# Optimization experiments

Measured on AMD Instinct MI355X. Metric: run time of the kernel, lower is better.

Reference implementation:

```python
import jax, jax.numpy as jnp
import numpy as np

H = 256
B = 4096          # number of graphs / motifs in batch
NF = 131072       # focal atoms
NR = 262144       # residues
V = 8001          # vocab.size() + 1
TOPK = 5
DIST_THRESH = 6.0


def setup_inputs() -> dict:
    key = jax.random.key(0)
    ks = jax.random.split(key, 12)
    h_ctx_focal = jax.random.normal(ks[0], (NF, H), dtype=jnp.float32)
    pos_ctx_focal = jax.random.normal(ks[1], (NF, 3), dtype=jnp.float32)
    current_wid = jax.random.randint(ks[2], (B,), 0, V)
    current_atoms_batch = jnp.sort(jax.random.randint(ks[3], (NF,), 0, B))
    h_residue = jax.random.normal(ks[4], (NR, H), dtype=jnp.float32)
    residue_pos = jax.random.normal(ks[5], (NR, 3, 3), dtype=jnp.float32)
    amino_acid_batch = jnp.sort(jax.random.randint(ks[6], (NR,), 0, B))
    emb_weight = jax.random.normal(ks[7], (V, H), dtype=jnp.float32) * 0.02
    mlp_w1 = jax.random.normal(ks[8], (3 * H, H), dtype=jnp.float32) * (1.0 / np.sqrt(3 * H))
    mlp_b1 = jnp.zeros((H,), dtype=jnp.float32)
    mlp_w2 = jax.random.normal(ks[9], (H, H), dtype=jnp.float32) * (1.0 / np.sqrt(H))
    mlp_b2 = jnp.zeros((H,), dtype=jnp.float32)
    return {
        'h_ctx_focal': h_ctx_focal, 'pos_ctx_focal': pos_ctx_focal,
        'current_wid': current_wid, 'current_atoms_batch': current_atoms_batch,
        'h_residue': h_residue, 'residue_pos': residue_pos,
        'amino_acid_batch': amino_acid_batch, 'emb_weight': emb_weight,
        'mlp_w1': mlp_w1, 'mlp_b1': mlp_b1, 'mlp_w2': mlp_w2, 'mlp_b2': mlp_b2,
    }


def reference(h_ctx_focal, pos_ctx_focal, current_wid, current_atoms_batch,
              h_residue, residue_pos, amino_acid_batch,
              emb_weight, mlp_w1, mlp_b1, mlp_w2, mlp_b2):
    nB = current_wid.shape[0]
    # scatter_add over focal atoms -> [B, H]
    node_hiddens = jax.ops.segment_sum(h_ctx_focal, current_atoms_batch, num_segments=nB)
    # embedding lookup -> [B, H]
    motif_hiddens = emb_weight[current_wid]
    # scatter_mean of positions -> [B, 3]
    pos_sum = jax.ops.segment_sum(pos_ctx_focal, current_atoms_batch, num_segments=nB)
    counts = jax.ops.segment_sum(jnp.ones((pos_ctx_focal.shape[0],), jnp.float32),
                                 current_atoms_batch, num_segments=nB)
    center_pos = pos_sum / jnp.maximum(counts, 1.0)[:, None]
    # CA position of each residue, distance mask (< 6 A from motif center)
    ca_pos = residue_pos[:, 1, :]                                  # [NR, 3]
    dist = jnp.linalg.norm(ca_pos - center_pos[amino_acid_batch], axis=1)
    mask = dist < DIST_THRESH                                      # [NR]
    # masked scatter_add of residue embeddings -> [B, H]
    residue_emb = jax.ops.segment_sum(jnp.where(mask[:, None], h_residue, 0.0),
                                      amino_acid_batch, num_segments=nB)
    # motif MLP (2 layers) + projection onto embedding table
    pred_vecs = jnp.concatenate([node_hiddens, motif_hiddens, residue_emb], axis=-1)  # [B, 3H]
    h = jax.nn.relu(pred_vecs @ mlp_w1 + mlp_b1)
    mh = h @ mlp_w2 + mlp_b2                                        # [B, H]
    pred_scores = mh @ emb_weight.T                                 # [B, V]
    # top-k + random selection among top-k
    _, select_pool = jax.lax.top_k(pred_scores, TOPK)               # [B, k]
    idx = jax.random.randint(jax.random.key(1), (nB,), 0, TOPK)
    preds = jnp.take_along_axis(select_pool, idx[:, None], axis=1)[:, 0]
    return (pred_scores, preds)
```

## Files before the change

kernel.cpp:

```cpp
#include <hip/hip_runtime.h>
#include <hip/hip_bf16.h>
#include <cstdint>

#define HD   256
#define BSZ  4096
#define NFV  131072
#define NRV  262144
#define VV   8001
#define TOPKN 5
#define RBOFF (BSZ + 1)
#define EPAD 8064

typedef __attribute__((ext_vector_type(8))) short short8v;
typedef __attribute__((ext_vector_type(4))) float float4v;

__host__ __device__ __forceinline__ unsigned rotl32(unsigned v, int d) {
  return (v << d) | (v >> (32 - d));
}

__host__ __device__ __forceinline__ void threefry2x32(
    unsigned k0, unsigned k1, unsigned x0, unsigned x1,
    unsigned& o0, unsigned& o1) {
  unsigned ks2 = k0 ^ k1 ^ 0x1BD11BDAu;
  x0 += k0; x1 += k1;
  x0 += x1; x1 = rotl32(x1, 13); x1 ^= x0;
  x0 += x1; x1 = rotl32(x1, 15); x1 ^= x0;
  x0 += x1; x1 = rotl32(x1, 26); x1 ^= x0;
  x0 += x1; x1 = rotl32(x1,  6); x1 ^= x0;
  x0 += k1; x1 += ks2 + 1u;
  x0 += x1; x1 = rotl32(x1, 17); x1 ^= x0;
  x0 += x1; x1 = rotl32(x1, 29); x1 ^= x0;
  x0 += x1; x1 = rotl32(x1, 16); x1 ^= x0;
  x0 += x1; x1 = rotl32(x1, 24); x1 ^= x0;
  x0 += ks2; x1 += k0 + 2u;
  x0 += x1; x1 = rotl32(x1, 13); x1 ^= x0;
  x0 += x1; x1 = rotl32(x1, 15); x1 ^= x0;
  x0 += x1; x1 = rotl32(x1, 26); x1 ^= x0;
  x0 += x1; x1 = rotl32(x1,  6); x1 ^= x0;
  x0 += k0; x1 += k1 + 3u;
  x0 += x1; x1 = rotl32(x1, 17); x1 ^= x0;
  x0 += x1; x1 = rotl32(x1, 29); x1 ^= x0;
  x0 += x1; x1 = rotl32(x1, 16); x1 ^= x0;
  x0 += x1; x1 = rotl32(x1, 24); x1 ^= x0;
  x0 += k1; x1 += ks2 + 4u;
  x0 += x1; x1 = rotl32(x1, 13); x1 ^= x0;
  x0 += x1; x1 = rotl32(x1, 15); x1 ^= x0;
  x0 += x1; x1 = rotl32(x1, 26); x1 ^= x0;
  x0 += x1; x1 = rotl32(x1,  6); x1 ^= x0;
  x0 += ks2; x1 += k0 + 5u;
  o0 = x0; o1 = x1;
}

__device__ __forceinline__ unsigned short f2bf(float f) {
  unsigned u = __float_as_uint(f);
  unsigned r = (u + 0x7FFFu + ((u >> 16) & 1u)) >> 16;
  return (unsigned short)r;
}
__device__ __forceinline__ float bf2f(unsigned short s) {
  return __uint_as_float(((unsigned)s) << 16);
}

__device__ __forceinline__ int lower_bound_i(const int* __restrict__ a, int n, int v) {
  int lo = 0, hi = n;
  while (lo < hi) { int m = (lo + hi) >> 1; if (a[m] < v) lo = m + 1; else hi = m; }
  return lo;
}

__device__ __forceinline__ void gl16(const unsigned short* g, unsigned short* l) {
  __builtin_amdgcn_global_load_lds(
      (const __attribute__((address_space(1))) unsigned int*)g,
      (__attribute__((address_space(3))) unsigned int*)l, 16, 0, 0);
}

__global__ __launch_bounds__(256) void prep_kernel(
    const int* __restrict__ ab, const int* __restrict__ rb, int* __restrict__ bounds,
    const float* __restrict__ emb, unsigned short* __restrict__ ehi,
    unsigned short* __restrict__ elo,
    const float* __restrict__ w1, unsigned short* __restrict__ w1th,
    unsigned short* __restrict__ w1tl,
    const float* __restrict__ w2, unsigned short* __restrict__ w2th,
    unsigned short* __restrict__ w2tl) {
  int blk = blockIdx.x, t = threadIdx.x;
  if (blk < 33) {
    int i = blk * 256 + t;
    if (i <= BSZ) bounds[i] = lower_bound_i(ab, NFV, i);
    else if (i <= 2 * BSZ + 1) bounds[i] = lower_bound_i(rb, NRV, i - RBOFF);
  } else if (blk < 33 + 2016) {
    size_t i = ((size_t)(blk - 33) * 256 + t) * 4;
    int row = (int)(i >> 8);
    float f[4] = {0.f, 0.f, 0.f, 0.f};
    if (row < VV) {
      float4 v = *reinterpret_cast<const float4*>(&emb[i]);
      f[0] = v.x; f[1] = v.y; f[2] = v.z; f[3] = v.w;
    }
    unsigned short h[4], l[4];
#pragma unroll
    for (int j = 0; j < 4; ++j) {
      h[j] = f2bf(f[j]);
      l[j] = f2bf(f[j] - bf2f(h[j]));
    }
    *reinterpret_cast<uint2*>(&ehi[i]) = *reinterpret_cast<uint2*>(h);
    *reinterpret_cast<uint2*>(&elo[i]) = *reinterpret_cast<uint2*>(l);
  } else if (blk < 33 + 2016 + 768) {
    int i = (blk - 2049) * 256 + t;
    int n = i / 768, k = i - n * 768;
    float v = w1[k * 256 + n];
    unsigned short h = f2bf(v);
    w1th[i] = h; w1tl[i] = f2bf(v - bf2f(h));
  } else {
    int i = (blk - 2817) * 256 + t;
    int n = i >> 8, k = i & 255;
    float v = w2[k * 256 + n];
    unsigned short h = f2bf(v);
    w2th[i] = h; w2tl[i] = f2bf(v - bf2f(h));
  }
}

__global__ __launch_bounds__(256) void mask_kernel(
    const float* __restrict__ pcf, const float* __restrict__ rpos,
    const int* __restrict__ bounds, unsigned char* __restrict__ mask) {
  int lane = threadIdx.x & 63;
  int b = blockIdx.x * 4 + (threadIdx.x >> 6);
  int a0 = bounds[b], a1 = bounds[b + 1];
  int r0 = bounds[RBOFF + b], r1 = bounds[RBOFF + b + 1];

  float cp = 0.f;
  if (lane < 3 && a0 < a1) {
    float nv = pcf[(size_t)a0 * 3 + lane];
    for (int aa = a0; aa < a1; ++aa) {
      float cv = nv;
      if (aa + 1 < a1) nv = pcf[(size_t)(aa + 1) * 3 + lane];
      cp += cv;
    }
  }
  if (lane < 3) cp = cp / fmaxf((float)(a1 - a0), 1.0f);
  float cx = __shfl(cp, 0), cy = __shfl(cp, 1), cz = __shfl(cp, 2);

  for (int r = r0 + lane; r < r1; r += 64) {
    float dx = rpos[(size_t)r * 9 + 3] - cx;
    float dy = rpos[(size_t)r * 9 + 4] - cy;
    float dz = rpos[(size_t)r * 9 + 5] - cz;
    mask[r] = (dx * dx + dy * dy + dz * dz < 36.0f) ? 1 : 0;
  }
}

__global__ __launch_bounds__(256) void fuse_seg_kernel(
    const float* __restrict__ hcf, const int* __restrict__ wid,
    const float* __restrict__ hres, const unsigned char* __restrict__ mask,
    const unsigned short* __restrict__ ehi, const unsigned short* __restrict__ elo,
    const int* __restrict__ bounds,
    unsigned short* __restrict__ pvh, unsigned short* __restrict__ pvl) {
  int lane = threadIdx.x & 63;
  int b = blockIdx.x * 4 + (threadIdx.x >> 6);
  int a0 = bounds[b], a1 = bounds[b + 1];
  int r0 = bounds[RBOFF + b], r1 = bounds[RBOFF + b + 1];
  size_t off = (size_t)lane * 4;

  float4v acc = 0.f;
  int a = a0;
  for (; a + 8 <= a1; a += 8) {
    float4v v[8];
#pragma unroll
    for (int j = 0; j < 8; ++j)
      v[j] = *reinterpret_cast<const float4v*>(&hcf[(size_t)(a + j) * HD + off]);
    acc += ((v[0] + v[1]) + (v[2] + v[3])) + ((v[4] + v[5]) + (v[6] + v[7]));
  }
  for (; a < a1; ++a)
    acc += *reinterpret_cast<const float4v*>(&hcf[(size_t)a * HD + off]);

  float4v racc = 0.f;
  int r = r0;
  for (; r < r1 && (r & 7); ++r) {
    float4v v = *reinterpret_cast<const float4v*>(&hres[(size_t)r * HD + off]);
    if (mask[r]) racc += v;
  }
  for (; r + 8 <= r1; r += 8) {
    uint2 mw = *reinterpret_cast<const uint2*>(&mask[r]);
    float4v v[8];
#pragma unroll
    for (int j = 0; j < 8; ++j)
      v[j] = *reinterpret_cast<const float4v*>(&hres[(size_t)(r + j) * HD + off]);
    float4v s0 = 0.f, s1 = 0.f, s2 = 0.f, s3 = 0.f;
    if (mw.x & 0x000000FFu) s0 += v[0];
    if (mw.x & 0x0000FF00u) s1 += v[1];
    if (mw.x & 0x00FF0000u) s2 += v[2];
    if (mw.x & 0xFF000000u) s3 += v[3];
    if (mw.y & 0x000000FFu) s0 += v[4];
    if (mw.y & 0x0000FF00u) s1 += v[5];
    if (mw.y & 0x00FF0000u) s2 += v[6];
    if (mw.y & 0xFF000000u) s3 += v[7];
    racc += (s0 + s1) + (s2 + s3);
  }
  for (; r < r1; ++r) {
    float4v v = *reinterpret_cast<const float4v*>(&hres[(size_t)r * HD + off]);
    if (mask[r]) racc += v;
  }

  size_t o = (size_t)b * 768;
  {
    unsigned short h[4], l[4];
#pragma unroll
    for (int j = 0; j < 4; ++j) {
      h[j] = f2bf(acc[j]); l[j] = f2bf(acc[j] - bf2f(h[j]));
    }
    *reinterpret_cast<uint2*>(&pvh[o + off]) = *reinterpret_cast<uint2*>(h);
    *reinterpret_cast<uint2*>(&pvl[o + off]) = *reinterpret_cast<uint2*>(l);
  }
  *reinterpret_cast<uint2*>(&pvh[o + 256 + off]) =
      *reinterpret_cast<const uint2*>(&ehi[(size_t)wid[b] * 256 + off]);
  *reinterpret_cast<uint2*>(&pvl[o + 256 + off]) =
      *reinterpret_cast<const uint2*>(&elo[(size_t)wid[b] * 256 + off]);
  {
    unsigned short h[4], l[4];
#pragma unroll
    for (int j = 0; j < 4; ++j) {
      h[j] = f2bf(racc[j]); l[j] = f2bf(racc[j] - bf2f(h[j]));
    }
    *reinterpret_cast<uint2*>(&pvh[o + 512 + off]) = *reinterpret_cast<uint2*>(h);
    *reinterpret_cast<uint2*>(&pvl[o + 512 + off]) = *reinterpret_cast<uint2*>(l);
  }
}

template <bool RELU, int K, int N>
__global__ __launch_bounds__(256) void mlp_gemm_kernel(
    const unsigned short* __restrict__ Ahg, const unsigned short* __restrict__ Alg,
    const unsigned short* __restrict__ Bhg, const unsigned short* __restrict__ Blg,
    const float* __restrict__ bias,
    unsigned short* __restrict__ Chi, unsigned short* __restrict__ Clo) {
  __shared__ __attribute__((aligned(16))) unsigned short Ahs[64][72];
  __shared__ __attribute__((aligned(16))) unsigned short Als[64][72];
  __shared__ __attribute__((aligned(16))) unsigned short Bhs[64][72];
  __shared__ __attribute__((aligned(16))) unsigned short Bls[64][72];

  int t = threadIdx.x;
  int bm = blockIdx.y * 64, bn = blockIdx.x * 64;
  int lane = t & 63, wv = t >> 6;
  int wm = wv >> 1, wn = wv & 1;
  int lr = lane & 15, lg = lane >> 4;
  float4v acc[2][2] = {};

  int srow = t >> 2, sc = (t & 3) * 16;

  for (int kb = 0; kb < K; kb += 64) {
    size_t ga = (size_t)(bm + srow) * K + kb + sc;
    size_t gb = (size_t)(bn + srow) * K + kb + sc;
    *reinterpret_cast<short8v*>(&Ahs[srow][sc]) = *reinterpret_cast<const short8v*>(&Ahg[ga]);
    *reinterpret_cast<short8v*>(&Ahs[srow][sc + 8]) = *reinterpret_cast<const short8v*>(&Ahg[ga + 8]);
    *reinterpret_cast<short8v*>(&Als[srow][sc]) = *reinterpret_cast<const short8v*>(&Alg[ga]);
    *reinterpret_cast<short8v*>(&Als[srow][sc + 8]) = *reinterpret_cast<const short8v*>(&Alg[ga + 8]);
    *reinterpret_cast<short8v*>(&Bhs[srow][sc]) = *reinterpret_cast<const short8v*>(&Bhg[gb]);
    *reinterpret_cast<short8v*>(&Bhs[srow][sc + 8]) = *reinterpret_cast<const short8v*>(&Bhg[gb + 8]);
    *reinterpret_cast<short8v*>(&Bls[srow][sc]) = *reinterpret_cast<const short8v*>(&Blg[gb]);
    *reinterpret_cast<short8v*>(&Bls[srow][sc + 8]) = *reinterpret_cast<const short8v*>(&Blg[gb + 8]);
    __syncthreads();

#pragma unroll
    for (int ks = 0; ks < 2; ++ks) {
      int ko = ks * 32 + lg * 8;
      short8v aH[2], aL[2], bH[2], bL[2];
#pragma unroll
      for (int f = 0; f < 2; ++f) {
        aH[f] = *reinterpret_cast<const short8v*>(&Ahs[wm * 32 + f * 16 + lr][ko]);
        aL[f] = *reinterpret_cast<const short8v*>(&Als[wm * 32 + f * 16 + lr][ko]);
        bH[f] = *reinterpret_cast<const short8v*>(&Bhs[wn * 32 + f * 16 + lr][ko]);
        bL[f] = *reinterpret_cast<const short8v*>(&Bls[wn * 32 + f * 16 + lr][ko]);
      }
#pragma unroll
      for (int mf = 0; mf < 2; ++mf)
#pragma unroll
        for (int nf = 0; nf < 2; ++nf) {
          acc[mf][nf] = __builtin_amdgcn_mfma_f32_16x16x32_bf16(
              aH[mf], bH[nf], acc[mf][nf], 0, 0, 0);
          acc[mf][nf] = __builtin_amdgcn_mfma_f32_16x16x32_bf16(
              aH[mf], bL[nf], acc[mf][nf], 0, 0, 0);
          acc[mf][nf] = __builtin_amdgcn_mfma_f32_16x16x32_bf16(
              aL[mf], bH[nf], acc[mf][nf], 0, 0, 0);
        }
    }
    __syncthreads();
  }

#pragma unroll
  for (int mf = 0; mf < 2; ++mf)
#pragma unroll
    for (int nf = 0; nf < 2; ++nf) {
      int col = bn + wn * 32 + nf * 16 + lr;
      float bv = bias[col];
#pragma unroll
      for (int rr = 0; rr < 4; ++rr) {
        int row = bm + wm * 32 + mf * 16 + lg * 4 + rr;
        float v = acc[mf][nf][rr] + bv;
        if (RELU) v = fmaxf(v, 0.f);
        unsigned short h = f2bf(v);
        Chi[(size_t)row * N + col] = h;
        Clo[(size_t)row * N + col] = f2bf(v - bf2f(h));
      }
    }
}

__global__ __launch_bounds__(256, 2) void score_gemm_kernel(
    const unsigned short* __restrict__ Ahg, const unsigned short* __restrict__ Alg,
    const unsigned short* __restrict__ Bhg, const unsigned short* __restrict__ Blg,
    float* __restrict__ C) {
  __shared__ __attribute__((aligned(16))) unsigned short Ah[128 * 64];
  __shared__ __attribute__((aligned(16))) unsigned short Al[128 * 64];
  __shared__ __attribute__((aligned(16))) unsigned short Bh[128 * 64];
  __shared__ __attribute__((aligned(16))) unsigned short Bl[128 * 64];

  int t = threadIdx.x;
  int bm = blockIdx.x * 128;
  int bn = blockIdx.y * 128;
  int lane = t & 63, wv = t >> 6;
  int wm = wv >> 1, wn = wv & 1;
  int lr = lane & 15, lg = lane >> 4;

  float4v acc[4][4] = {};

  int rsub = lane >> 3;
  int cb = (lane & 7) * 16;

  for (int kb = 0; kb < 256; kb += 64) {
#pragma unroll
    for (int j = 0; j < 4; ++j) {
      int ch = wv * 4 + j;
      int grow = ch * 8 + rsub;
      int scb = cb ^ ((grow & 7) << 4);
      size_t goA = (size_t)(bm + grow) * 256 + kb + (scb >> 1);
      size_t goB = (size_t)(bn + grow) * 256 + kb + (scb >> 1);
      unsigned lo = ch * 512 + lane * 8;
      gl16(&Ahg[goA], &Ah[lo]);
      gl16(&Alg[goA], &Al[lo]);
      gl16(&Bhg[goB], &Bh[lo]);
      gl16(&Blg[goB], &Bl[lo]);
    }
    __syncthreads();

#pragma unroll
    for (int ks = 0; ks < 2; ++ks) {
      int bo = (ks * 32 + lg * 8) * 2;
      short8v aH[4], aL[4], bH[4], bL[4];
#pragma unroll
      for (int f = 0; f < 4; ++f) {
        int ra = wm * 64 + f * 16 + lr;
        int rb2 = wn * 64 + f * 16 + lr;
        int oa = ra * 128 + (bo ^ ((ra & 7) << 4));
        int ob2 = rb2 * 128 + (bo ^ ((rb2 & 7) << 4));
        aH[f] = *reinterpret_cast<const short8v*>((const char*)Ah + oa);
        aL[f] = *reinterpret_cast<const short8v*>((const char*)Al + oa);
        bH[f] = *reinterpret_cast<const short8v*>((const char*)Bh + ob2);
        bL[f] = *reinterpret_cast<const short8v*>((const char*)Bl + ob2);
      }
#pragma unroll
      for (int mf = 0; mf < 4; ++mf)
#pragma unroll
        for (int nf = 0; nf < 4; ++nf) {
          acc[mf][nf] = __builtin_amdgcn_mfma_f32_16x16x32_bf16(
              aH[mf], bH[nf], acc[mf][nf], 0, 0, 0);
          acc[mf][nf] = __builtin_amdgcn_mfma_f32_16x16x32_bf16(
              aH[mf], bL[nf], acc[mf][nf], 0, 0, 0);
          acc[mf][nf] = __builtin_amdgcn_mfma_f32_16x16x32_bf16(
              aL[mf], bH[nf], acc[mf][nf], 0, 0, 0);
        }
    }
    __syncthreads();
  }

#pragma unroll
  for (int mf = 0; mf < 4; ++mf)
#pragma unroll
    for (int nf = 0; nf < 4; ++nf) {
      int col = bn + wn * 64 + nf * 16 + lr;
      if (col < VV) {
#pragma unroll
        for (int rr = 0; rr < 4; ++rr) {
          int row = bm + wm * 64 + mf * 16 + lg * 4 + rr;
          C[(size_t)row * VV + col] = acc[mf][nf][rr];
        }
      }
    }
}

#define BETTER(av, ai, bv, bi) ((av) > (bv) || ((av) == (bv) && (ai) < (bi)))

__global__ __launch_bounds__(256) void topk_kernel(
    const float* __restrict__ scores, float* __restrict__ preds,
    unsigned k1a, unsigned k1b, unsigned k2a, unsigned k2b) {
  int lane = threadIdx.x & 63;
  int row = (blockIdx.x << 2) + (threadIdx.x >> 6);
  const float* s = scores + (size_t)row * VV;

  const float NEG = -__builtin_huge_valf();
  float v0 = NEG, v1 = NEG, v2 = NEG, v3 = NEG, v4 = NEG;
  int i0 = 0x7FFFFFFF, i1 = 0x7FFFFFFF, i2 = 0x7FFFFFFF, i3 = 0x7FFFFFFF, i4 = 0x7FFFFFFF;

  for (int v = lane; v < VV; v += 64) {
    float val = s[v];
    if (BETTER(val, v, v4, i4)) {
      if (BETTER(val, v, v3, i3)) {
        v4 = v3; i4 = i3;
        if (BETTER(val, v, v2, i2)) {
          v3 = v2; i3 = i2;
          if (BETTER(val, v, v1, i1)) {
            v2 = v1; i2 = i1;
            if (BETTER(val, v, v0, i0)) {
              v1 = v0; i1 = i0; v0 = val; i0 = v;
            } else { v1 = val; i1 = v; }
          } else { v2 = val; i2 = v; }
        } else { v3 = val; i3 = v; }
      } else { v4 = val; i4 = v; }
    }
  }

  int sel0, sel1, sel2, sel3, sel4;
#pragma unroll
  for (int p = 0; p < TOPKN; ++p) {
    float bv = v0; int bi = i0;
#pragma unroll
    for (int off = 32; off > 0; off >>= 1) {
      float ov = __shfl_xor(bv, off);
      int   oi = __shfl_xor(bi, off);
      if (BETTER(ov, oi, bv, bi)) { bv = ov; bi = oi; }
    }
    if (p == 0) sel0 = bi; else if (p == 1) sel1 = bi; else if (p == 2) sel2 = bi;
    else if (p == 3) sel3 = bi; else sel4 = bi;
    if (bi == i0) {
      v0 = v1; i0 = i1; v1 = v2; i1 = i2; v2 = v3; i2 = i3; v3 = v4; i3 = i4;
      v4 = NEG; i4 = 0x7FFFFFFF;
    }
  }

  if (lane == 0) {
    unsigned i = (unsigned)row;
    unsigned h0, h1, l0, l1;
    threefry2x32(k1a, k1b, 0u, i, h0, h1);
    threefry2x32(k2a, k2b, 0u, i, l0, l1);
    unsigned idx = (((h0 ^ h1) % 5u) + ((l0 ^ l1) % 5u)) % 5u;
    int pick = (idx == 0) ? sel0 : (idx == 1) ? sel1 : (idx == 2) ? sel2
             : (idx == 3) ? sel3 : sel4;
    preds[row] = (float)pick;
  }
}

extern "C" void kernel_launch(void* const* d_in, const int* in_sizes, int n_in,
                              void* d_out, int out_size, void* d_ws, size_t ws_size,
                              hipStream_t stream) {
  const float* hcf  = (const float*)d_in[0];
  const float* pcf  = (const float*)d_in[1];
  const int*   wid  = (const int*)d_in[2];
  const int*   ab   = (const int*)d_in[3];
  const float* hres = (const float*)d_in[4];
  const float* rpos = (const float*)d_in[5];
  const int*   rb   = (const int*)d_in[6];
  const float* emb  = (const float*)d_in[7];
  const float* w1   = (const float*)d_in[8];
  const float* bb1  = (const float*)d_in[9];
  const float* w2   = (const float*)d_in[10];
  const float* bb2  = (const float*)d_in[11];

  float* out    = (float*)d_out;
  float* scores = out;
  float* preds  = out + (size_t)BSZ * VV;

  char* ob = (char*)d_out;
  unsigned short* pvh  = (unsigned short*)(ob);
  unsigned short* pvl  = (unsigned short*)(ob + 0x600000);
  unsigned short* hh   = (unsigned short*)(ob + 0xC00000);
  unsigned short* hl   = (unsigned short*)(ob + 0xE00000);
  unsigned short* w1th = (unsigned short*)(ob + 0x1000000);
  unsigned short* w1tl = (unsigned short*)(ob + 0x1060000);
  unsigned short* w2th = (unsigned short*)(ob + 0x10C0000);
  unsigned short* w2tl = (unsigned short*)(ob + 0x10E0000);

  char* ws = (char*)d_ws;
  int*            bounds = (int*)(ws);
  unsigned char*  mask   = (unsigned char*)(ws + 0x10000);
  unsigned short* mh_hi  = (unsigned short*)(ws + 0x100000);
  unsigned short* mh_lo  = (unsigned short*)(ws + 0x300000);
  unsigned short* emb_hi = (unsigned short*)(ws + 0x500000);
  unsigned short* emb_lo = (unsigned short*)(ws + 0x900000);

  prep_kernel<<<33 + 2016 + 768 + 256, 256, 0, stream>>>(
      ab, rb, bounds, emb, emb_hi, emb_lo, w1, w1th, w1tl, w2, w2th, w2tl);

  mask_kernel<<<BSZ / 4, 256, 0, stream>>>(pcf, rpos, bounds, mask);

  fuse_seg_kernel<<<BSZ / 4, 256, 0, stream>>>(
      hcf, wid, hres, mask, emb_hi, emb_lo, bounds, pvh, pvl);

  mlp_gemm_kernel<true, 768, 256><<<dim3(4, 64), 256, 0, stream>>>(
      pvh, pvl, w1th, w1tl, bb1, hh, hl);
  mlp_gemm_kernel<false, 256, 256><<<dim3(4, 64), 256, 0, stream>>>(
      hh, hl, w2th, w2tl, bb2, mh_hi, mh_lo);

  score_gemm_kernel<<<dim3(BSZ / 128, EPAD / 128), 256, 0, stream>>>(
      mh_hi, mh_lo, emb_hi, emb_lo, scores);

  unsigned k1a, k1b, k2a, k2b;
  threefry2x32(0u, 1u, 0u, 0u, k1a, k1b);
  threefry2x32(0u, 1u, 0u, 1u, k2a, k2b);
  topk_kernel<<<BSZ / 4, 256, 0, stream>>>(scores, preds, k1a, k1b, k2a, k2b);
}
```

Before: 293.2 us.

## Split each segment's row reduction across two wavefronts with LDS combine

The segment-sum kernel now assigns two wavefronts per graph instead of one. Each wavefront accumulates alternating 8-row chunks of the focal and residue features, and the partial sums are combined through shared memory before the hi/lo bf16 split is written. The aim is more memory-level parallelism and shorter per-wave serial chains in this bandwidth-bound reduction. The cost is twice the blocks, extra __syncthreads barriers, and an LDS round trip.

```diff
diff --git a/kernel.cpp b/kernel.cpp
--- a/kernel.cpp
+++ b/kernel.cpp
@@ -150,71 +150,94 @@
     const unsigned short* __restrict__ ehi, const unsigned short* __restrict__ elo,
     const int* __restrict__ bounds,
     unsigned short* __restrict__ pvh, unsigned short* __restrict__ pvl) {
-  int lane = threadIdx.x & 63;
-  int b = blockIdx.x * 4 + (threadIdx.x >> 6);
+  int t = threadIdx.x;
+  int lane = t & 63, wv = t >> 6;
+  int half = wv & 1;
+  int b = blockIdx.x * 2 + (wv >> 1);
   int a0 = bounds[b], a1 = bounds[b + 1];
   int r0 = bounds[RBOFF + b], r1 = bounds[RBOFF + b + 1];
   size_t off = (size_t)lane * 4;
+  size_t o = (size_t)b * 768;
+
+  __shared__ float4v part[4][64];
 
   float4v acc = 0.f;
-  int a = a0;
-  for (; a + 8 <= a1; a += 8) {
-    float4v v[8];
-#pragma unroll
-    for (int j = 0; j < 8; ++j)
-      v[j] = *reinterpret_cast<const float4v*>(&hcf[(size_t)(a + j) * HD + off]);
-    acc += ((v[0] + v[1]) + (v[2] + v[3])) + ((v[4] + v[5]) + (v[6] + v[7]));
-  }
-  for (; a < a1; ++a)
-    acc += *reinterpret_cast<const float4v*>(&hcf[(size_t)a * HD + off]);
-
-  float4v racc = 0.f;
-  int r = r0;
-  for (; r < r1 && (r & 7); ++r) {
-    float4v v = *reinterpret_cast<const float4v*>(&hres[(size_t)r * HD + off]);
-    if (mask[r]) racc += v;
-  }
-  for (; r + 8 <= r1; r += 8) {
-    uint2 mw = *reinterpret_cast<const uint2*>(&mask[r]);
-    float4v v[8];
-#pragma unroll
-    for (int j = 0; j < 8; ++j)
-      v[j] = *reinterpret_cast<const float4v*>(&hres[(size_t)(r + j) * HD + off]);
-    float4v s0 = 0.f, s1 = 0.f, s2 = 0.f, s3 = 0.f;
-    if (mw.x & 0x000000FFu) s0 += v[0];
-    if (mw.x & 0x0000FF00u) s1 += v[1];
-    if (mw.x & 0x00FF0000u) s2 += v[2];
-    if (mw.x & 0xFF000000u) s3 += v[3];
-    if (mw.y & 0x000000FFu) s0 += v[4];
-    if (mw.y & 0x0000FF00u) s1 += v[5];
-    if (mw.y & 0x00FF0000u) s2 += v[6];
-    if (mw.y & 0xFF000000u) s3 += v[7];
-    racc += (s0 + s1) + (s2 + s3);
-  }
-  for (; r < r1; ++r) {
-    float4v v = *reinterpret_cast<const float4v*>(&hres[(size_t)r * HD + off]);
-    if (mask[r]) racc += v;
-  }
-
-  size_t o = (size_t)b * 768;
-  {
+  for (int c = half;; c += 2) {
+    int base = a0 + 8 * c;
+    if (base >= a1) break;
+    if (base + 8 <= a1) {
+      float4v v[8];
+#pragma unroll
+      for (int j = 0; j < 8; ++j)
+        v[j] = *reinterpret_cast<const float4v*>(&hcf[(size_t)(base + j) * HD + off]);
+      acc += ((v[0] + v[1]) + (v[2] + v[3])) + ((v[4] + v[5]) + (v[6] + v[7]));
+    } else {
+      for (int a = base; a < a1; ++a)
+        acc += *reinterpret_cast<const float4v*>(&hcf[(size_t)a * HD + off]);
+    }
+  }
+  part[wv][lane] = acc;
+  __syncthreads();
+  if (half == 0) {
+    float4v s = part[wv][lane] + part[wv + 1][lane];
     unsigned short h[4], l[4];
 #pragma unroll
     for (int j = 0; j < 4; ++j) {
-      h[j] = f2bf(acc[j]); l[j] = f2bf(acc[j] - bf2f(h[j]));
+      h[j] = f2bf(s[j]); l[j] = f2bf(s[j] - bf2f(h[j]));
     }
     *reinterpret_cast<uint2*>(&pvh[o + off]) = *reinterpret_cast<uint2*>(h);
     *reinterpret_cast<uint2*>(&pvl[o + off]) = *reinterpret_cast<uint2*>(l);
-  }
-  *reinterpret_cast<uint2*>(&pvh[o + 256 + off]) =
-      *reinterpret_cast<const uint2*>(&ehi[(size_t)wid[b] * 256 + off]);
-  *reinterpret_cast<uint2*>(&pvl[o + 256 + off]) =
-      *reinterpret_cast<const uint2*>(&elo[(size_t)wid[b] * 256 + off]);
-  {
+  } else {
+    *reinterpret_cast<uint2*>(&pvh[o + 256 + off]) =
+        *reinterpret_cast<const uint2*>(&ehi[(size_t)wid[b] * 256 + off]);
+    *reinterpret_cast<uint2*>(&pvl[o + 256 + off]) =
+        *reinterpret_cast<const uint2*>(&elo[(size_t)wid[b] * 256 + off]);
+  }
+  __syncthreads();
+
+  float4v racc = 0.f;
+  int ra = (r0 + 7) & ~7;
+  if (half == 0) {
+    int pe = ra < r1 ? ra : r1;
+    for (int r = r0; r < pe; ++r) {
+      float4v v = *reinterpret_cast<const float4v*>(&hres[(size_t)r * HD + off]);
+      if (mask[r]) racc += v;
+    }
+  }
+  for (int c = half;; c += 2) {
+    int base = ra + 8 * c;
+    if (base >= r1) break;
+    if (base + 8 <= r1) {
+      uint2 mw = *reinterpret_cast<const uint2*>(&mask[base]);
+      float4v v[8];
+#pragma unroll
+      for (int j = 0; j < 8; ++j)
+        v[j] = *reinterpret_cast<const float4v*>(&hres[(size_t)(base + j) * HD + off]);
+      float4v s0 = 0.f, s1 = 0.f, s2 = 0.f, s3 = 0.f;
+      if (mw.x & 0x000000FFu) s0 += v[0];
+      if (mw.x & 0x0000FF00u) s1 += v[1];
+      if (mw.x & 0x00FF0000u) s2 += v[2];
+      if (mw.x & 0xFF000000u) s3 += v[3];
+      if (mw.y & 0x000000FFu) s0 += v[4];
+      if (mw.y & 0x0000FF00u) s1 += v[5];
+      if (mw.y & 0x00FF0000u) s2 += v[6];
+      if (mw.y & 0xFF000000u) s3 += v[7];
+      racc += (s0 + s1) + (s2 + s3);
+    } else {
+      for (int r = base; r < r1; ++r) {
+        float4v v = *reinterpret_cast<const float4v*>(&hres[(size_t)r * HD + off]);
+        if (mask[r]) racc += v;
+      }
+    }
+  }
+  part[wv][lane] = racc;
+  __syncthreads();
+  if (half == 0) {
+    float4v s = part[wv][lane] + part[wv + 1][lane];
     unsigned short h[4], l[4];
 #pragma unroll
     for (int j = 0; j < 4; ++j) {
-      h[j] = f2bf(racc[j]); l[j] = f2bf(racc[j] - bf2f(h[j]));
+      h[j] = f2bf(s[j]); l[j] = f2bf(s[j] - bf2f(h[j]));
     }
     *reinterpret_cast<uint2*>(&pvh[o + 512 + off]) = *reinterpret_cast<uint2*>(h);
     *reinterpret_cast<uint2*>(&pvl[o + 512 + off]) = *reinterpret_cast<uint2*>(l);
@@ -484,7 +507,7 @@
 
   mask_kernel<<<BSZ / 4, 256, 0, stream>>>(pcf, rpos, bounds, mask);
 
-  fuse_seg_kernel<<<BSZ / 4, 256, 0, stream>>>(
+  fuse_seg_kernel<<<BSZ / 2, 256, 0, stream>>>(
       hcf, wid, hres, mask, emb_hi, emb_lo, bounds, pvh, pvl);
 
   mlp_gemm_kernel<true, 768, 256><<<dim3(4, 64), 256, 0, stream>>>(
```

After: 291.4 us. No clear change (-0.6%).
